# Optimization experiments

Hardware: AMD Instinct MI355X
Metric: run time of the kernel (lower is better)

The kernel has to match this reference:

```python
import jax, jax.numpy as jnp
import numpy as np
import math

MARGIN = 0.3
SCALE = 30.0
NUM_CLASSES = 100000
EMB_DIM = 512
BATCH = 1024


def setup_inputs() -> dict:
    key = jax.random.key(0)
    k1, k2, k3 = jax.random.split(key, 3)
    embeddings = jax.random.normal(k1, (BATCH, EMB_DIM), dtype=jnp.float32)
    labels = jax.random.randint(k2, (BATCH,), 0, NUM_CLASSES, dtype=jnp.int64)
    # xavier_uniform for weight [num_classes, embedding_dim]
    limit = math.sqrt(6.0 / (NUM_CLASSES + EMB_DIM))
    weight = jax.random.uniform(k3, (NUM_CLASSES, EMB_DIM), dtype=jnp.float32,
                                minval=-limit, maxval=limit)
    return {"embeddings": embeddings, "labels": labels, "weight": weight}


def reference(embeddings, labels, weight):
    cos_m = math.cos(MARGIN)
    sin_m = math.sin(MARGIN)
    th = math.cos(math.pi - MARGIN)
    mm = math.sin(math.pi - MARGIN) * MARGIN

    # normalize weight rows only (embeddings are NOT normalized in the original)
    w_norm = weight / jnp.linalg.norm(weight, axis=1, keepdims=True)
    cosine = jnp.einsum('bd,cd->bc', embeddings, w_norm)  # [B, C]
    sine = jnp.sqrt(jnp.clip(1.0 - cosine * cosine, 0.0, 1.0))
    phi = cosine * cos_m - sine * sin_m
    phi = jnp.where(cosine > th, phi, cosine - mm)

    one_hot = jax.nn.one_hot(labels, cosine.shape[1], dtype=cosine.dtype)
    logits = SCALE * (one_hot * phi + (1.0 - one_hot) * cosine)

    logp = jax.nn.log_softmax(logits, axis=-1)
    nll = -jnp.take_along_axis(logp, labels[:, None], axis=1)[:, 0]
    return jnp.mean(nll)
```

## Files before the change

kernel.cpp:

```cpp
#include <hip/hip_runtime.h>
#include <math.h>

#define B_N 1024
#define D_K 512
#define C_N 100000
#define SCALEF 30.0f
#define COS_M 0.9553364891256061f
#define SIN_M 0.29552020666133955f
#define TH_C (-0.9553364891256061f)
#define MM_C 0.08865606199840186f
#define FIXM 160.0f

#define BM 128
#define BN 128
#define BK 64
#define NCT ((C_N + BN - 1) / BN)
#define NCTP 784

typedef short bf16x8 __attribute__((ext_vector_type(8)));
typedef float f32x4  __attribute__((ext_vector_type(4)));

__device__ inline unsigned bf16rne(float f) {
    unsigned u = __float_as_uint(f);
    u += 0x7fffu + ((u >> 16) & 1u);
    return u >> 16;
}
__device__ inline unsigned pk2(float lo, float hi) {
    return bf16rne(lo) | (bf16rne(hi) << 16);
}

__device__ static __forceinline__ void async16(const void* g, void* l) {
    __builtin_amdgcn_global_load_lds(
        (const __attribute__((address_space(1))) unsigned int*)g,
        (__attribute__((address_space(3))) unsigned int*)l, 16, 0, 0);
}

__global__ __launch_bounds__(256) void prep_kernel(
    const float* __restrict__ w, unsigned short* __restrict__ wbf,
    const float* __restrict__ e, unsigned short* __restrict__ ebf,
    float* __restrict__ gacc)
{
    int bid = blockIdx.x;
    if (bid < 25000) {
        int wave = threadIdx.x >> 6;
        int lane = threadIdx.x & 63;
        int c = bid * 4 + wave;
        const float4* p = (const float4*)(w + (size_t)c * D_K);
        float4 a = p[lane];
        float4 b = p[lane + 64];
        float s = a.x*a.x + a.y*a.y + a.z*a.z + a.w*a.w
                + b.x*b.x + b.y*b.y + b.z*b.z + b.w*b.w;
        #pragma unroll
        for (int off = 32; off; off >>= 1) s += __shfl_xor(s, off, 64);
        float rn = 1.0f / sqrtf(s);
        uint2 o0, o1;
        o0.x = pk2(a.x * rn, a.y * rn); o0.y = pk2(a.z * rn, a.w * rn);
        o1.x = pk2(b.x * rn, b.y * rn); o1.y = pk2(b.z * rn, b.w * rn);
        uint2* q = (uint2*)(wbf + (size_t)c * D_K);
        q[lane] = o0;
        q[lane + 64] = o1;
    } else if (bid < 25512) {
        int i = (bid - 25000) * 256 + threadIdx.x;
        float4 v = ((const float4*)e)[i];
        uint2 o;
        o.x = pk2(v.x, v.y);
        o.y = pk2(v.z, v.w);
        ((uint2*)ebf)[i] = o;
    } else {
        float4 z = make_float4(0.f, 0.f, 0.f, 0.f);
        ((float4*)gacc)[threadIdx.x] = z;
    }
}

__global__ __launch_bounds__(256) void gemm_lse_kernel(
    const unsigned short* __restrict__ ebf, const unsigned short* __restrict__ wbf,
    const int* __restrict__ labels,
    float* __restrict__ gacc, float* __restrict__ target)
{
    __shared__ short As[BM * BK];
    __shared__ short Bs[BN * BK];
    __shared__ int   labS[BM];

    const int bid = blockIdx.x;
    const int g8 = bid >> 6, r8 = (bid >> 3) & 7, j8 = bid & 7;
    const int ct = g8 * 8 + j8;
    const int rt = r8;
    const int row0 = rt * BM;
    const int col0 = ct * BN;
    const int t = threadIdx.x;
    const int lane = t & 63, wave = t >> 6;
    const int wx = wave & 1, wy = wave >> 1;
    const int lc = lane & 15, q = lane >> 4;

    if (t < BM) labS[t] = labels[row0 + t];
    __syncthreads();

    const int srow = t >> 3;
    const int sslot = t & 7;
    const int gch = (sslot - srow) & 7;
    const unsigned short* aptr = ebf + (size_t)(row0 + srow) * D_K + gch * 8;
    int bR[4];
    #pragma unroll
    for (int p = 0; p < 4; ++p) {
        int br = col0 + 32 * p + srow;
        bR[p] = (br < C_N) ? br : (C_N - 1);
    }
    const unsigned short* bptr[4] = {
        wbf + (size_t)bR[0] * D_K + gch * 8, wbf + (size_t)bR[1] * D_K + gch * 8,
        wbf + (size_t)bR[2] * D_K + gch * 8, wbf + (size_t)bR[3] * D_K + gch * 8 };
    short* ldsA = As + t * 8;
    short* ldsB = Bs + t * 8;

    f32x4 acc[4][4] = {};

    for (int it = 0; it < D_K / BK; ++it) {
        const int k0 = it * BK;
        __syncthreads();
        #pragma unroll
        for (int p = 0; p < 4; ++p)
            async16(aptr + (size_t)32 * p * D_K + k0, ldsA + p * 2048);
        #pragma unroll
        for (int p = 0; p < 4; ++p)
            async16(bptr[p] + k0, ldsB + p * 2048);
        __syncthreads();

        #pragma unroll
        for (int kh = 0; kh < 2; ++kh) {
            bf16x8 aF[4], bF[4];
            #pragma unroll
            for (int si = 0; si < 4; ++si) {
                int r = wy * 64 + si * 16 + lc;
                int slot = (kh * 4 + q + r) & 7;
                aF[si] = *(const bf16x8*)(As + r * BK + slot * 8);
            }
            #pragma unroll
            for (int sj = 0; sj < 4; ++sj) {
                int r = wx * 64 + sj * 16 + lc;
                int slot = (kh * 4 + q + r) & 7;
                bF[sj] = *(const bf16x8*)(Bs + r * BK + slot * 8);
            }
            #pragma unroll
            for (int si = 0; si < 4; ++si)
                #pragma unroll
                for (int sj = 0; sj < 4; ++sj)
                    acc[si][sj] = __builtin_amdgcn_mfma_f32_16x16x32_bf16(
                        aF[si], bF[sj], acc[si][sj], 0, 0, 0);
        }
    }

    #pragma unroll
    for (int si = 0; si < 4; ++si) {
        #pragma unroll
        for (int reg = 0; reg < 4; ++reg) {
            int rl = wy * 64 + si * 16 + q * 4 + reg;
            int lab = labS[rl];
            float s = 0.0f;
            #pragma unroll
            for (int sj = 0; sj < 4; ++sj) {
                int cg = col0 + wx * 64 + sj * 16 + lc;
                float cosv = acc[si][sj][reg];
                float v;
                if (cg == lab) {
                    float sine = sqrtf(fminf(fmaxf(1.0f - cosv * cosv, 0.0f), 1.0f));
                    float phi = cosv * COS_M - sine * SIN_M;
                    phi = (cosv > TH_C) ? phi : (cosv - MM_C);
                    v = SCALEF * phi;
                    target[row0 + rl] = v;
                } else {
                    v = SCALEF * cosv;
                }
                if (cg < C_N) s += __expf(v - FIXM);
            }
            #pragma unroll
            for (int off = 1; off < 16; off <<= 1)
                s += __shfl_xor(s, off, 64);
            if (lc == 0) atomicAdd(&gacc[row0 + rl], s);
        }
    }
}

__global__ __launch_bounds__(1024) void finish_kernel(
    const float* __restrict__ gacc, const float* __restrict__ target,
    float* __restrict__ out)
{
    int t = threadIdx.x;
    float v = (FIXM + logf(gacc[t])) - target[t];
    #pragma unroll
    for (int off = 1; off < 64; off <<= 1) v += __shfl_xor(v, off, 64);
    __shared__ float ws[16];
    int wave = t >> 6, lane = t & 63;
    if (lane == 0) ws[wave] = v;
    __syncthreads();
    if (t == 0) {
        float sum = 0.f;
        for (int w = 0; w < 16; ++w) sum += ws[w];
        out[0] = sum / (float)B_N;
    }
}

__global__ __launch_bounds__(256) void prep_fb_kernel(
    const float* __restrict__ w, float* __restrict__ rnorm,
    const float* __restrict__ e, unsigned short* __restrict__ ebf,
    float* __restrict__ gacc)
{
    int bid = blockIdx.x;
    if (bid < 25000) {
        int wave = threadIdx.x >> 6;
        int lane = threadIdx.x & 63;
        int c = bid * 4 + wave;
        const float4* p = (const float4*)(w + (size_t)c * D_K);
        float4 a = p[lane];
        float4 b = p[lane + 64];
        float s = a.x*a.x + a.y*a.y + a.z*a.z + a.w*a.w
                + b.x*b.x + b.y*b.y + b.z*b.z + b.w*b.w;
        #pragma unroll
        for (int off = 32; off; off >>= 1) s += __shfl_xor(s, off, 64);
        if (lane == 0) rnorm[c] = 1.0f / sqrtf(s);
    } else if (bid < 25512) {
        int i = (bid - 25000) * 256 + threadIdx.x;
        float4 v = ((const float4*)e)[i];
        uint2 o;
        o.x = pk2(v.x, v.y);
        o.y = pk2(v.z, v.w);
        ((uint2*)ebf)[i] = o;
    } else {
        float4 z = make_float4(0.f, 0.f, 0.f, 0.f);
        ((float4*)gacc)[threadIdx.x] = z;
    }
}

#define ROWS 40
__global__ __launch_bounds__(256) void gemm_lse_fb_kernel(
    const unsigned short* __restrict__ ebf, const float* __restrict__ wgt,
    const int* __restrict__ labels, const float* __restrict__ rnorm,
    float* __restrict__ gacc, float* __restrict__ target)
{
    __shared__ short As[BM * ROWS];
    __shared__ short Bs[BN * ROWS];
    __shared__ float rnS[BN];
    __shared__ int   labS[BM];

    const int rt = blockIdx.x;
    const int ct = blockIdx.y;
    const int row0 = rt * BM;
    const int col0 = ct * BN;
    const int t = threadIdx.x;
    const int lane = t & 63, wave = t >> 6;
    const int wx = wave & 1, wy = wave >> 1;
    const int lc = lane & 15, q = lane >> 4;

    if (t < BN) {
        int c = col0 + t;
        rnS[t] = (c < C_N) ? rnorm[c] : 0.0f;
    } else {
        labS[t - BN] = labels[row0 + (t - BN)];
    }
    __syncthreads();

    const int sr = t >> 1;
    const int sh = t & 1;
    const int cB = col0 + sr;
    const bool bval = cB < C_N;
    const float rn = rnS[sr];
    const unsigned short* aptr = ebf + (size_t)(row0 + sr) * D_K + sh * 16;
    const float* bptr0 = wgt + (size_t)(bval ? cB : 0) * D_K + sh * 16;

    f32x4 acc[4][4] = {};

    for (int it = 0; it < D_K / 32; ++it) {
        const int k0 = it * 32;
        uint4 a0 = ((const uint4*)(aptr + k0))[0];
        uint4 a1 = ((const uint4*)(aptr + k0))[1];
        float4 b0 = make_float4(0.f,0.f,0.f,0.f), b1 = b0, b2 = b0, b3 = b0;
        if (bval) {
            const float4* bp = (const float4*)(bptr0 + k0);
            b0 = bp[0]; b1 = bp[1]; b2 = bp[2]; b3 = bp[3];
        }
        uint4 w0, w1;
        w0.x = pk2(b0.x * rn, b0.y * rn); w0.y = pk2(b0.z * rn, b0.w * rn);
        w0.z = pk2(b1.x * rn, b1.y * rn); w0.w = pk2(b1.z * rn, b1.w * rn);
        w1.x = pk2(b2.x * rn, b2.y * rn); w1.y = pk2(b2.z * rn, b2.w * rn);
        w1.z = pk2(b3.x * rn, b3.y * rn); w1.w = pk2(b3.z * rn, b3.w * rn);

        __syncthreads();
        *(uint4*)(As + sr * ROWS + sh * 16)     = a0;
        *(uint4*)(As + sr * ROWS + sh * 16 + 8) = a1;
        *(uint4*)(Bs + sr * ROWS + sh * 16)     = w0;
        *(uint4*)(Bs + sr * ROWS + sh * 16 + 8) = w1;
        __syncthreads();

        bf16x8 aF[4], bF[4];
        #pragma unroll
        for (int si = 0; si < 4; ++si)
            aF[si] = *(const bf16x8*)(As + (wy * 64 + si * 16 + lc) * ROWS + q * 8);
        #pragma unroll
        for (int sj = 0; sj < 4; ++sj)
            bF[sj] = *(const bf16x8*)(Bs + (wx * 64 + sj * 16 + lc) * ROWS + q * 8);
        #pragma unroll
        for (int si = 0; si < 4; ++si)
            #pragma unroll
            for (int sj = 0; sj < 4; ++sj)
                acc[si][sj] = __builtin_amdgcn_mfma_f32_16x16x32_bf16(
                    aF[si], bF[sj], acc[si][sj], 0, 0, 0);
    }

    #pragma unroll
    for (int si = 0; si < 4; ++si) {
        #pragma unroll
        for (int reg = 0; reg < 4; ++reg) {
            int rl = wy * 64 + si * 16 + q * 4 + reg;
            int lab = labS[rl];
            float s = 0.0f;
            #pragma unroll
            for (int sj = 0; sj < 4; ++sj) {
                int cg = col0 + wx * 64 + sj * 16 + lc;
                float cosv = acc[si][sj][reg];
                float v;
                if (cg == lab) {
                    float sine = sqrtf(fminf(fmaxf(1.0f - cosv * cosv, 0.0f), 1.0f));
                    float phi = cosv * COS_M - sine * SIN_M;
                    phi = (cosv > TH_C) ? phi : (cosv - MM_C);
                    v = SCALEF * phi;
                    target[row0 + rl] = v;
                } else {
                    v = SCALEF * cosv;
                }
                if (cg < C_N) s += __expf(v - FIXM);
            }
            #pragma unroll
            for (int off = 1; off < 16; off <<= 1)
                s += __shfl_xor(s, off, 64);
            if (lc == 0) atomicAdd(&gacc[row0 + rl], s);
        }
    }
}

extern "C" void kernel_launch(void* const* d_in, const int* in_sizes, int n_in,
                              void* d_out, int out_size, void* d_ws, size_t ws_size,
                              hipStream_t stream) {
    const float* emb    = (const float*)d_in[0];
    const int*   labels = (const int*)d_in[1];
    const float* wgt    = (const float*)d_in[2];
    float* out = (float*)d_out;
    char* ws = (char*)d_ws;

    if (ws_size >= 103456768ull) {
        float* gacc          = (float*)(ws);
        float* target        = (float*)(ws + 4096);
        unsigned short* ebf  = (unsigned short*)(ws + 8192);
        unsigned short* wbf  = (unsigned short*)(ws + 1056768);

        prep_kernel<<<25513, 256, 0, stream>>>(wgt, wbf, emb, ebf, gacc);
        gemm_lse_kernel<<<(NCTP / 8) * 64, 256, 0, stream>>>(ebf, wbf, labels, gacc, target);
        finish_kernel<<<1, 1024, 0, stream>>>(gacc, target, out);
    } else {
        float* gacc          = (float*)(ws);
        float* target        = (float*)(ws + 4096);
        unsigned short* ebf  = (unsigned short*)(ws + 8192);
        float* rnorm         = (float*)(ws + 1056768);

        prep_fb_kernel<<<25513, 256, 0, stream>>>(wgt, rnorm, emb, ebf, gacc);
        dim3 gridB(B_N / BM, NCT);
        gemm_lse_fb_kernel<<<gridB, 256, 0, stream>>>(ebf, wgt, labels, rnorm, gacc, target);
        finish_kernel<<<1, 1024, 0, stream>>>(gacc, target, out);
    }
}
```

Before: 489.3 us.

## Switch main GEMM path to FP8 with exact label logit and partial-sum reduction

The main path now quantizes normalized weights (scaled by 16) and embeddings (scaled by 4) to FP8 and runs the GEMM with fp8 MFMA over a K-tile of 128. This halves the bytes of the intermediate weight copy and doubles MFMA throughput. The label logit is computed exactly in fp32 in the prep kernel and swapped into the sum, so the FP8 error in the target term is corrected. Per-tile row sums are written to a partial buffer instead of atomics and reduced by a new per-row kernel, at the cost of extra partial traffic and FP8 accuracy risk in the softmax denominator.

New measurement: 407.9 us. 16.6% less time.

```diff
diff --git a/kernel.cpp b/kernel.cpp
--- a/kernel.cpp
+++ b/kernel.cpp
@@ -13,7 +13,6 @@
 
 #define BM 128
 #define BN 128
-#define BK 64
 #define NCT ((C_N + BN - 1) / BN)
 #define NCTP 784
 
@@ -28,6 +27,11 @@
 __device__ inline unsigned pk2(float lo, float hi) {
     return bf16rne(lo) | (bf16rne(hi) << 16);
 }
+__device__ inline int pkf8(float a, float b, float c, float d) {
+    int r = __builtin_amdgcn_cvt_pk_fp8_f32(a, b, 0, false);
+    r = __builtin_amdgcn_cvt_pk_fp8_f32(c, d, r, true);
+    return r;
+}
 
 __device__ static __forceinline__ void async16(const void* g, void* l) {
     __builtin_amdgcn_global_load_lds(
@@ -36,7 +40,197 @@
 }
 
 __global__ __launch_bounds__(256) void prep_kernel(
-    const float* __restrict__ w, unsigned short* __restrict__ wbf,
+    const float* __restrict__ w, unsigned char* __restrict__ wq8,
+    const float* __restrict__ e, unsigned char* __restrict__ eq8,
+    const int* __restrict__ labels, float* __restrict__ texact,
+    float* __restrict__ out)
+{
+    int bid = blockIdx.x;
+    int wave = threadIdx.x >> 6;
+    int lane = threadIdx.x & 63;
+    if (bid < 25000) {
+        int c = bid * 4 + wave;
+        const float4* p = (const float4*)(w + (size_t)c * D_K);
+        float4 a = p[lane];
+        float4 b = p[lane + 64];
+        float s = a.x*a.x + a.y*a.y + a.z*a.z + a.w*a.w
+                + b.x*b.x + b.y*b.y + b.z*b.z + b.w*b.w;
+        #pragma unroll
+        for (int off = 32; off; off >>= 1) s += __shfl_xor(s, off, 64);
+        float rn = 16.0f / sqrtf(s);
+        int o0 = pkf8(a.x * rn, a.y * rn, a.z * rn, a.w * rn);
+        int o1 = pkf8(b.x * rn, b.y * rn, b.z * rn, b.w * rn);
+        int* q = (int*)(wq8 + (size_t)c * D_K);
+        q[lane] = o0;
+        q[lane + 64] = o1;
+    } else if (bid < 25128) {
+        int i = (bid - 25000) * 256 + threadIdx.x;
+        const float4* p = ((const float4*)e) + i * 4;
+        float4 v0 = p[0], v1 = p[1], v2 = p[2], v3 = p[3];
+        int4 o;
+        o.x = pkf8(v0.x * 4.f, v0.y * 4.f, v0.z * 4.f, v0.w * 4.f);
+        o.y = pkf8(v1.x * 4.f, v1.y * 4.f, v1.z * 4.f, v1.w * 4.f);
+        o.z = pkf8(v2.x * 4.f, v2.y * 4.f, v2.z * 4.f, v2.w * 4.f);
+        o.w = pkf8(v3.x * 4.f, v3.y * 4.f, v3.z * 4.f, v3.w * 4.f);
+        ((int4*)eq8)[i] = o;
+    } else if (bid < 25384) {
+        int b = (bid - 25128) * 4 + wave;
+        int lab = labels[b];
+        const float4* pe = (const float4*)(e + (size_t)b * D_K);
+        const float4* pw = (const float4*)(w + (size_t)lab * D_K);
+        float4 e0 = pe[lane], e1 = pe[lane + 64];
+        float4 w0 = pw[lane], w1 = pw[lane + 64];
+        float dot = e0.x*w0.x + e0.y*w0.y + e0.z*w0.z + e0.w*w0.w
+                  + e1.x*w1.x + e1.y*w1.y + e1.z*w1.z + e1.w*w1.w;
+        float nrm = w0.x*w0.x + w0.y*w0.y + w0.z*w0.z + w0.w*w0.w
+                  + w1.x*w1.x + w1.y*w1.y + w1.z*w1.z + w1.w*w1.w;
+        #pragma unroll
+        for (int off = 32; off; off >>= 1) {
+            dot += __shfl_xor(dot, off, 64);
+            nrm += __shfl_xor(nrm, off, 64);
+        }
+        if (lane == 0) {
+            float cosv = dot / sqrtf(nrm);
+            float sine = sqrtf(fminf(fmaxf(1.0f - cosv * cosv, 0.0f), 1.0f));
+            float phi = cosv * COS_M - sine * SIN_M;
+            phi = (cosv > TH_C) ? phi : (cosv - MM_C);
+            texact[b] = SCALEF * phi;
+        }
+    } else {
+        if (threadIdx.x == 0) out[0] = 0.0f;
+    }
+}
+
+__global__ __launch_bounds__(256) void gemm_lse_kernel(
+    const unsigned char* __restrict__ eq8, const unsigned char* __restrict__ wq8,
+    const int* __restrict__ labels,
+    float* __restrict__ partial, float* __restrict__ labraw)
+{
+    __shared__ unsigned char As[BM * 128];
+    __shared__ unsigned char Bs[BN * 128];
+    __shared__ int   labS[BM];
+    __shared__ float sS[BM][2];
+
+    const int bid = blockIdx.x;
+    const int g8 = bid >> 6, r8 = (bid >> 3) & 7, j8 = bid & 7;
+    const int ct = g8 * 8 + j8;
+    const int row0 = r8 * BM;
+    const int col0 = ct * BN;
+    const int t = threadIdx.x;
+    const int lane = t & 63, wave = t >> 6;
+    const int wx = wave & 1, wy = wave >> 1;
+    const int lc = lane & 15, q = lane >> 4;
+
+    if (t < BM) labS[t] = labels[row0 + t];
+    __syncthreads();
+
+    const int srow = t >> 3;
+    const int sslot = t & 7;
+    const int gch = (sslot - srow) & 7;
+    const unsigned char* aptr = eq8 + (size_t)(row0 + srow) * D_K + gch * 16;
+    int bR[4];
+    #pragma unroll
+    for (int p = 0; p < 4; ++p) {
+        int br = col0 + 32 * p + srow;
+        bR[p] = (br < C_N) ? br : (C_N - 1);
+    }
+    const unsigned char* bptr[4] = {
+        wq8 + (size_t)bR[0] * D_K + gch * 16, wq8 + (size_t)bR[1] * D_K + gch * 16,
+        wq8 + (size_t)bR[2] * D_K + gch * 16, wq8 + (size_t)bR[3] * D_K + gch * 16 };
+    unsigned char* ldsA = As + t * 16;
+    unsigned char* ldsB = Bs + t * 16;
+
+    f32x4 acc[4][4] = {};
+
+    for (int it = 0; it < 4; ++it) {
+        const int k0 = it * 128;
+        __syncthreads();
+        #pragma unroll
+        for (int p = 0; p < 4; ++p)
+            async16(aptr + (size_t)32 * p * D_K + k0, ldsA + p * 4096);
+        #pragma unroll
+        for (int p = 0; p < 4; ++p)
+            async16(bptr[p] + k0, ldsB + p * 4096);
+        __syncthreads();
+
+        #pragma unroll
+        for (int kh = 0; kh < 4; ++kh) {
+            long aF[4], bF[4];
+            const int c16 = kh * 2 + (q >> 1);
+            const int h8 = (q & 1) * 8;
+            #pragma unroll
+            for (int si = 0; si < 4; ++si) {
+                int r = wy * 64 + si * 16 + lc;
+                int slot = (c16 + r) & 7;
+                aF[si] = *(const long*)(As + r * 128 + slot * 16 + h8);
+            }
+            #pragma unroll
+            for (int sj = 0; sj < 4; ++sj) {
+                int r = wx * 64 + sj * 16 + lc;
+                int slot = (c16 + r) & 7;
+                bF[sj] = *(const long*)(Bs + r * 128 + slot * 16 + h8);
+            }
+            #pragma unroll
+            for (int si = 0; si < 4; ++si)
+                #pragma unroll
+                for (int sj = 0; sj < 4; ++sj)
+                    acc[si][sj] = __builtin_amdgcn_mfma_f32_16x16x32_fp8_fp8(
+                        aF[si], bF[sj], acc[si][sj], 0, 0, 0);
+        }
+    }
+
+    const float LSC = SCALEF / 64.0f;
+    #pragma unroll
+    for (int si = 0; si < 4; ++si) {
+        #pragma unroll
+        for (int reg = 0; reg < 4; ++reg) {
+            int rl = wy * 64 + si * 16 + q * 4 + reg;
+            int lab = labS[rl];
+            float s = 0.0f;
+            #pragma unroll
+            for (int sj = 0; sj < 4; ++sj) {
+                int cg = col0 + wx * 64 + sj * 16 + lc;
+                float lv = acc[si][sj][reg] * LSC;
+                if (cg == lab) labraw[row0 + rl] = lv;
+                if (cg < C_N) s += __expf(lv - FIXM);
+            }
+            #pragma unroll
+            for (int off = 1; off < 16; off <<= 1)
+                s += __shfl_xor(s, off, 64);
+            if (lc == 0) sS[rl][wx] = s;
+        }
+    }
+    __syncthreads();
+    if (t < BM)
+        partial[(size_t)ct * B_N + row0 + t] = sS[t][0] + sS[t][1];
+}
+
+__global__ __launch_bounds__(256) void reduce_kernel(
+    const float* __restrict__ partial, const float* __restrict__ labraw,
+    const float* __restrict__ texact, float* __restrict__ out)
+{
+    int b = blockIdx.x;
+    int t = threadIdx.x;
+    float s = 0.0f;
+    #pragma unroll
+    for (int ct = t; ct < NCTP; ct += 256) s += partial[(size_t)ct * B_N + b];
+    #pragma unroll
+    for (int off = 1; off < 64; off <<= 1) s += __shfl_xor(s, off, 64);
+    __shared__ float ss[4];
+    int wave = t >> 6, lane = t & 63;
+    if (lane == 0) ss[wave] = s;
+    __syncthreads();
+    if (t == 0) {
+        float stot = ss[0] + ss[1] + ss[2] + ss[3];
+        float te = texact[b];
+        stot += __expf(te - FIXM) - __expf(labraw[b] - FIXM);
+        float nll = (FIXM + logf(stot)) - te;
+        atomicAdd(out, nll * (1.0f / (float)B_N));
+    }
+}
+
+__global__ __launch_bounds__(256) void prep_fb_kernel(
+    const float* __restrict__ w, float* __restrict__ rnorm,
     const float* __restrict__ e, unsigned short* __restrict__ ebf,
     float* __restrict__ gacc)
 {
@@ -52,13 +246,7 @@
                 + b.x*b.x + b.y*b.y + b.z*b.z + b.w*b.w;
         #pragma unroll
         for (int off = 32; off; off >>= 1) s += __shfl_xor(s, off, 64);
-        float rn = 1.0f / sqrtf(s);
-        uint2 o0, o1;
-        o0.x = pk2(a.x * rn, a.y * rn); o0.y = pk2(a.z * rn, a.w * rn);
-        o1.x = pk2(b.x * rn, b.y * rn); o1.y = pk2(b.z * rn, b.w * rn);
-        uint2* q = (uint2*)(wbf + (size_t)c * D_K);
-        q[lane] = o0;
-        q[lane + 64] = o1;
+        if (lane == 0) rnorm[c] = 1.0f / sqrtf(s);
     } else if (bid < 25512) {
         int i = (bid - 25000) * 256 + threadIdx.x;
         float4 v = ((const float4*)e)[i];
@@ -72,19 +260,19 @@
     }
 }
 
-__global__ __launch_bounds__(256) void gemm_lse_kernel(
-    const unsigned short* __restrict__ ebf, const unsigned short* __restrict__ wbf,
-    const int* __restrict__ labels,
+#define ROWS 40
+__global__ __launch_bounds__(256) void gemm_lse_fb_kernel(
+    const unsigned short* __restrict__ ebf, const float* __restrict__ wgt,
+    const int* __restrict__ labels, const float* __restrict__ rnorm,
     float* __restrict__ gacc, float* __restrict__ target)
 {
-    __shared__ short As[BM * BK];
-    __shared__ short Bs[BN * BK];
+    __shared__ short As[BM * ROWS];
+    __shared__ short Bs[BN * ROWS];
+    __shared__ float rnS[BN];
     __shared__ int   labS[BM];
 
-    const int bid = blockIdx.x;
-    const int g8 = bid >> 6, r8 = (bid >> 3) & 7, j8 = bid & 7;
-    const int ct = g8 * 8 + j8;
-    const int rt = r8;
+    const int rt = blockIdx.x;
+    const int ct = blockIdx.y;
     const int row0 = rt * BM;
     const int col0 = ct * BN;
     const int t = threadIdx.x;
@@ -92,60 +280,59 @@
     const int wx = wave & 1, wy = wave >> 1;
     const int lc = lane & 15, q = lane >> 4;
 
-    if (t < BM) labS[t] = labels[row0 + t];
+    if (t < BN) {
+        int c = col0 + t;
+        rnS[t] = (c < C_N) ? rnorm[c] : 0.0f;
+    } else {
+        labS[t - BN] = labels[row0 + (t - BN)];
+    }
     __syncthreads();
 
-    const int srow = t >> 3;
-    const int sslot = t & 7;
-    const int gch = (sslot - srow) & 7;
-    const unsigned short* aptr = ebf + (size_t)(row0 + srow) * D_K + gch * 8;
-    int bR[4];
-    #pragma unroll
-    for (int p = 0; p < 4; ++p) {
-        int br = col0 + 32 * p + srow;
-        bR[p] = (br < C_N) ? br : (C_N - 1);
-    }
-    const unsigned short* bptr[4] = {
-        wbf + (size_t)bR[0] * D_K + gch * 8, wbf + (size_t)bR[1] * D_K + gch * 8,
-        wbf + (size_t)bR[2] * D_K + gch * 8, wbf + (size_t)bR[3] * D_K + gch * 8 };
-    short* ldsA = As + t * 8;
-    short* ldsB = Bs + t * 8;
+    const int sr = t >> 1;
+    const int sh = t & 1;
+    const int cB = col0 + sr;
+    const bool bval = cB < C_N;
+    const float rn = rnS[sr];
+    const unsigned short* aptr = ebf + (size_t)(row0 + sr) * D_K + sh * 16;
+    const float* bptr0 = wgt + (size_t)(bval ? cB : 0) * D_K + sh * 16;
 
     f32x4 acc[4][4] = {};
 
-    for (int it = 0; it < D_K / BK; ++it) {
-        const int k0 = it * BK;
+    for (int it = 0; it < D_K / 32; ++it) {
+        const int k0 = it * 32;
+        uint4 a0 = ((const uint4*)(aptr + k0))[0];
+        uint4 a1 = ((const uint4*)(aptr + k0))[1];
+        float4 b0 = make_float4(0.f,0.f,0.f,0.f), b1 = b0, b2 = b0, b3 = b0;
+        if (bval) {
+            const float4* bp = (const float4*)(bptr0 + k0);
+            b0 = bp[0]; b1 = bp[1]; b2 = bp[2]; b3 = bp[3];
+        }
+        uint4 w0, w1;
+        w0.x = pk2(b0.x * rn, b0.y * rn); w0.y = pk2(b0.z * rn, b0.w * rn);
+        w0.z = pk2(b1.x * rn, b1.y * rn); w0.w = pk2(b1.z * rn, b1.w * rn);
+        w1.x = pk2(b2.x * rn, b2.y * rn); w1.y = pk2(b2.z * rn, b2.w * rn);
+        w1.z = pk2(b3.x * rn, b3.y * rn); w1.w = pk2(b3.z * rn, b3.w * rn);
+
         __syncthreads();
-        #pragma unroll
-        for (int p = 0; p < 4; ++p)
-            async16(aptr + (size_t)32 * p * D_K + k0, ldsA + p * 2048);
-        #pragma unroll
-        for (int p = 0; p < 4; ++p)
-            async16(bptr[p] + k0, ldsB + p * 2048);
+        *(uint4*)(As + sr * ROWS + sh * 16)     = a0;
+        *(uint4*)(As + sr * ROWS + sh * 16 + 8) = a1;
+        *(uint4*)(Bs + sr * ROWS + sh * 16)     = w0;
+        *(uint4*)(Bs + sr * ROWS + sh * 16 + 8) = w1;
         __syncthreads();
 
-        #pragma unroll
-        for (int kh = 0; kh < 2; ++kh) {
-            bf16x8 aF[4], bF[4];
-            #pragma unroll
-            for (int si = 0; si < 4; ++si) {
-                int r = wy * 64 + si * 16 + lc;
-                int slot = (kh * 4 + q + r) & 7;
-                aF[si] = *(const bf16x8*)(As + r * BK + slot * 8);
-            }
-            #pragma unroll
-            for (int sj = 0; sj < 4; ++sj) {
-                int r = wx * 64 + sj * 16 + lc;
-                int slot = (kh * 4 + q + r) & 7;
-                bF[sj] = *(const bf16x8*)(Bs + r * BK + slot * 8);
-            }
-            #pragma unroll
-            for (int si = 0; si < 4; ++si)
-                #pragma unroll
-                for (int sj = 0; sj < 4; ++sj)
-                    acc[si][sj] = __builtin_amdgcn_mfma_f32_16x16x32_bf16(
-                        aF[si], bF[sj], acc[si][sj], 0, 0, 0);
-        }
+        bf16x8 aF[4], bF[4];
+        #pragma unroll
+        for (int si = 0; si < 4; ++si)
+            aF[si] = *(const bf16x8*)(As + (wy * 64 + si * 16 + lc) * ROWS + q * 8);
+        #pragma unroll
+        for (int sj = 0; sj < 4; ++sj)
+            bF[sj] = *(const bf16x8*)(Bs + (wx * 64 + sj * 16 + lc) * ROWS + q * 8);
+        #pragma unroll
+        for (int si = 0; si < 4; ++si)
+            #pragma unroll
+            for (int sj = 0; sj < 4; ++sj)
+                acc[si][sj] = __builtin_amdgcn_mfma_f32_16x16x32_bf16(
+                    aF[si], bF[sj], acc[si][sj], 0, 0, 0);
     }
 
     #pragma unroll
@@ -179,7 +366,7 @@
     }
 }
 
-__global__ __launch_bounds__(1024) void finish_kernel(
+__global__ __launch_bounds__(1024) void finish_fb_kernel(
     const float* __restrict__ gacc, const float* __restrict__ target,
     float* __restrict__ out)
 {
@@ -198,143 +385,6 @@
     }
 }
 
-__global__ __launch_bounds__(256) void prep_fb_kernel(
-    const float* __restrict__ w, float* __restrict__ rnorm,
-    const float* __restrict__ e, unsigned short* __restrict__ ebf,
-    float* __restrict__ gacc)
-{
-    int bid = blockIdx.x;
-    if (bid < 25000) {
-        int wave = threadIdx.x >> 6;
-        int lane = threadIdx.x & 63;
-        int c = bid * 4 + wave;
-        const float4* p = (const float4*)(w + (size_t)c * D_K);
-        float4 a = p[lane];
-        float4 b = p[lane + 64];
-        float s = a.x*a.x + a.y*a.y + a.z*a.z + a.w*a.w
-                + b.x*b.x + b.y*b.y + b.z*b.z + b.w*b.w;
-        #pragma unroll
-        for (int off = 32; off; off >>= 1) s += __shfl_xor(s, off, 64);
-        if (lane == 0) rnorm[c] = 1.0f / sqrtf(s);
-    } else if (bid < 25512) {
-        int i = (bid - 25000) * 256 + threadIdx.x;
-        float4 v = ((const float4*)e)[i];
-        uint2 o;
-        o.x = pk2(v.x, v.y);
-        o.y = pk2(v.z, v.w);
-        ((uint2*)ebf)[i] = o;
-    } else {
-        float4 z = make_float4(0.f, 0.f, 0.f, 0.f);
-        ((float4*)gacc)[threadIdx.x] = z;
-    }
-}
-
-#define ROWS 40
-__global__ __launch_bounds__(256) void gemm_lse_fb_kernel(
-    const unsigned short* __restrict__ ebf, const float* __restrict__ wgt,
-    const int* __restrict__ labels, const float* __restrict__ rnorm,
-    float* __restrict__ gacc, float* __restrict__ target)
-{
-    __shared__ short As[BM * ROWS];
-    __shared__ short Bs[BN * ROWS];
-    __shared__ float rnS[BN];
-    __shared__ int   labS[BM];
-
-    const int rt = blockIdx.x;
-    const int ct = blockIdx.y;
-    const int row0 = rt * BM;
-    const int col0 = ct * BN;
-    const int t = threadIdx.x;
-    const int lane = t & 63, wave = t >> 6;
-    const int wx = wave & 1, wy = wave >> 1;
-    const int lc = lane & 15, q = lane >> 4;
-
-    if (t < BN) {
-        int c = col0 + t;
-        rnS[t] = (c < C_N) ? rnorm[c] : 0.0f;
-    } else {
-        labS[t - BN] = labels[row0 + (t - BN)];
-    }
-    __syncthreads();
-
-    const int sr = t >> 1;
-    const int sh = t & 1;
-    const int cB = col0 + sr;
-    const bool bval = cB < C_N;
-    const float rn = rnS[sr];
-    const unsigned short* aptr = ebf + (size_t)(row0 + sr) * D_K + sh * 16;
-    const float* bptr0 = wgt + (size_t)(bval ? cB : 0) * D_K + sh * 16;
-
-    f32x4 acc[4][4] = {};
-
-    for (int it = 0; it < D_K / 32; ++it) {
-        const int k0 = it * 32;
-        uint4 a0 = ((const uint4*)(aptr + k0))[0];
-        uint4 a1 = ((const uint4*)(aptr + k0))[1];
-        float4 b0 = make_float4(0.f,0.f,0.f,0.f), b1 = b0, b2 = b0, b3 = b0;
-        if (bval) {
-            const float4* bp = (const float4*)(bptr0 + k0);
-            b0 = bp[0]; b1 = bp[1]; b2 = bp[2]; b3 = bp[3];
-        }
-        uint4 w0, w1;
-        w0.x = pk2(b0.x * rn, b0.y * rn); w0.y = pk2(b0.z * rn, b0.w * rn);
-        w0.z = pk2(b1.x * rn, b1.y * rn); w0.w = pk2(b1.z * rn, b1.w * rn);
-        w1.x = pk2(b2.x * rn, b2.y * rn); w1.y = pk2(b2.z * rn, b2.w * rn);
-        w1.z = pk2(b3.x * rn, b3.y * rn); w1.w = pk2(b3.z * rn, b3.w * rn);
-
-        __syncthreads();
-        *(uint4*)(As + sr * ROWS + sh * 16)     = a0;
-        *(uint4*)(As + sr * ROWS + sh * 16 + 8) = a1;
-        *(uint4*)(Bs + sr * ROWS + sh * 16)     = w0;
-        *(uint4*)(Bs + sr * ROWS + sh * 16 + 8) = w1;
-        __syncthreads();
-
-        bf16x8 aF[4], bF[4];
-        #pragma unroll
-        for (int si = 0; si < 4; ++si)
-            aF[si] = *(const bf16x8*)(As + (wy * 64 + si * 16 + lc) * ROWS + q * 8);
-        #pragma unroll
-        for (int sj = 0; sj < 4; ++sj)
-            bF[sj] = *(const bf16x8*)(Bs + (wx * 64 + sj * 16 + lc) * ROWS + q * 8);
-        #pragma unroll
-        for (int si = 0; si < 4; ++si)
-            #pragma unroll
-            for (int sj = 0; sj < 4; ++sj)
-                acc[si][sj] = __builtin_amdgcn_mfma_f32_16x16x32_bf16(
-                    aF[si], bF[sj], acc[si][sj], 0, 0, 0);
-    }
-
-    #pragma unroll
-    for (int si = 0; si < 4; ++si) {
-        #pragma unroll
-        for (int reg = 0; reg < 4; ++reg) {
-            int rl = wy * 64 + si * 16 + q * 4 + reg;
-            int lab = labS[rl];
-            float s = 0.0f;
-            #pragma unroll
-            for (int sj = 0; sj < 4; ++sj) {
-                int cg = col0 + wx * 64 + sj * 16 + lc;
-                float cosv = acc[si][sj][reg];
-                float v;
-                if (cg == lab) {
-                    float sine = sqrtf(fminf(fmaxf(1.0f - cosv * cosv, 0.0f), 1.0f));
-                    float phi = cosv * COS_M - sine * SIN_M;
-                    phi = (cosv > TH_C) ? phi : (cosv - MM_C);
-                    v = SCALEF * phi;
-                    target[row0 + rl] = v;
-                } else {
-                    v = SCALEF * cosv;
-                }
-                if (cg < C_N) s += __expf(v - FIXM);
-            }
-            #pragma unroll
-            for (int off = 1; off < 16; off <<= 1)
-                s += __shfl_xor(s, off, 64);
-            if (lc == 0) atomicAdd(&gacc[row0 + rl], s);
-        }
-    }
-}
-
 extern "C" void kernel_launch(void* const* d_in, const int* in_sizes, int n_in,
                               void* d_out, int out_size, void* d_ws, size_t ws_size,
                               hipStream_t stream) {
@@ -344,15 +394,16 @@
     float* out = (float*)d_out;
     char* ws = (char*)d_ws;
 
-    if (ws_size >= 103456768ull) {
-        float* gacc          = (float*)(ws);
-        float* target        = (float*)(ws + 4096);
-        unsigned short* ebf  = (unsigned short*)(ws + 8192);
-        unsigned short* wbf  = (unsigned short*)(ws + 1056768);
-
-        prep_kernel<<<25513, 256, 0, stream>>>(wgt, wbf, emb, ebf, gacc);
-        gemm_lse_kernel<<<(NCTP / 8) * 64, 256, 0, stream>>>(ebf, wbf, labels, gacc, target);
-        finish_kernel<<<1, 1024, 0, stream>>>(gacc, target, out);
+    if (ws_size >= 56000000ull) {
+        float* texact        = (float*)(ws);
+        float* labraw        = (float*)(ws + 4096);
+        float* partial       = (float*)(ws + 8192);
+        unsigned char* eq8   = (unsigned char*)(ws + 3219456);
+        unsigned char* wq8   = (unsigned char*)(ws + 3743744);
+
+        prep_kernel<<<25385, 256, 0, stream>>>(wgt, wq8, emb, eq8, labels, texact, out);
+        gemm_lse_kernel<<<(NCTP / 8) * 64, 256, 0, stream>>>(eq8, wq8, labels, partial, labraw);
+        reduce_kernel<<<B_N, 256, 0, stream>>>(partial, labraw, texact, out);
     } else {
         float* gacc          = (float*)(ws);
         float* target        = (float*)(ws + 4096);
@@ -362,6 +413,6 @@
         prep_fb_kernel<<<25513, 256, 0, stream>>>(wgt, rnorm, emb, ebf, gacc);
         dim3 gridB(B_N / BM, NCT);
         gemm_lse_fb_kernel<<<gridB, 256, 0, stream>>>(ebf, wgt, labels, rnorm, gacc, target);
-        finish_kernel<<<1, 1024, 0, stream>>>(gacc, target, out);
-    }
-}
+        finish_fb_kernel<<<1, 1024, 0, stream>>>(gacc, target, out);
+    }
+}
```
